# Kernel optimization log

Hardware: AMD Instinct MI355X
Metric: run time of the kernel (lower is better)

## Reference

```python
import jax, jax.numpy as jnp
import numpy as np

B, S, D_IN, D_OUT, N_EXPERTS = 8, 4096, 512, 512, 8


def setup_inputs() -> dict:
    key = jax.random.key(0)
    k1, k2, k3, k4 = jax.random.split(key, 4)
    x = jax.random.normal(k1, (B, S, D_IN), dtype=jnp.float32)
    partitions = jax.random.randint(k2, (B, S), 0, N_EXPERTS, dtype=jnp.int32)
    # per-branch nn.Linear weights: [n, out_features, in_features], kaiming-ish scale
    W = jax.random.normal(k3, (N_EXPERTS, D_OUT, D_IN), dtype=jnp.float32) * 0.03
    b = jax.random.normal(k4, (N_EXPERTS, D_OUT), dtype=jnp.float32) * 0.01
    return {"x": x, "partitions": partitions, "W": W, "b": b}


def reference(x, partitions, W, b):
    # Hard token partition -> per-branch linear -> scatter combine.
    # Equivalent math to dynamic_partition + branch Linear + dynamic_stitch:
    # out[t] = x[t] @ W[p[t]].T + b[p[t]]
    in_shape = x.shape
    xf = x.reshape(-1, in_shape[-1])          # [T, d_in]
    p = partitions.reshape(-1)                # [T]
    # Compute all-expert outputs, then select per-token expert (vectorized
    # replacement for the variable-size per-partition GEMM loop).
    y = jnp.einsum('td,eod->teo', xf, W) + b[None, :, :]   # [T, n, d_out]
    out = jnp.take_along_axis(y, p[:, None, None], axis=1)[:, 0, :]  # [T, d_out]
    return out.reshape(in_shape[:-1] + (W.shape[1],))
```

## Files before the change

kernel.cpp:

```cpp
#include <hip/hip_runtime.h>
#include <hip/hip_bf16.h>

#define N_EXPERTS 8
#define T_TOKENS 32768
#define D 512
#define TILE 128
#define BK 64
#define MAX_MTILES 264
#define SORT_CAP (MAX_MTILES * TILE)
#define NT (D / TILE)
#define GRID_WG (NT * MAX_MTILES)

typedef __bf16 bf16x8 __attribute__((ext_vector_type(8)));
typedef float  f32x4  __attribute__((ext_vector_type(4)));
typedef unsigned short u16x8 __attribute__((ext_vector_type(8)));

__device__ __forceinline__ unsigned short f2bf(float f) {
    unsigned int u = __float_as_uint(f);
    u += 0x7FFFu + ((u >> 16) & 1u);
    return (unsigned short)(u >> 16);
}

__device__ __forceinline__ u16x8 ldcvt8(const float* p) {
    float4 a = *(const float4*)p;
    float4 b = *(const float4*)(p + 4);
    u16x8 o;
    o[0] = f2bf(a.x); o[1] = f2bf(a.y); o[2] = f2bf(a.z); o[3] = f2bf(a.w);
    o[4] = f2bf(b.x); o[5] = f2bf(b.y); o[6] = f2bf(b.z); o[7] = f2bf(b.w);
    return o;
}

__device__ __forceinline__ void gl2lds16(const void* g, void* l) {
    __builtin_amdgcn_global_load_lds(
        (const __attribute__((address_space(1))) void*)g,
        (__attribute__((address_space(3))) void*)l, 16, 0, 0);
}

__global__ void hist_kernel(const int* __restrict__ p, int* __restrict__ counts) {
    __shared__ int h[N_EXPERTS];
    int tid = threadIdx.x;
    if (tid < N_EXPERTS) h[tid] = 0;
    __syncthreads();
    for (int t = blockIdx.x * blockDim.x + tid; t < T_TOKENS; t += gridDim.x * blockDim.x)
        atomicAdd(&h[p[t]], 1);
    __syncthreads();
    if (tid < N_EXPERTS) atomicAdd(&counts[tid], h[tid]);
}

__global__ void scatter_kernel(const int* __restrict__ p, const int* __restrict__ counts,
                               int* __restrict__ fill, int* __restrict__ sorted) {
    __shared__ int lcount[N_EXPERTS];
    __shared__ int lbase[N_EXPERTS];
    __shared__ int sps[N_EXPERTS];
    int tid = threadIdx.x;
    if (tid < N_EXPERTS) lcount[tid] = 0;
    __syncthreads();
    int t = blockIdx.x * blockDim.x + tid;
    int e = 0, lrank = 0;
    if (t < T_TOKENS) {
        e = p[t];
        lrank = atomicAdd(&lcount[e], 1);
    }
    __syncthreads();
    if (tid < N_EXPERTS)
        lbase[tid] = (lcount[tid] > 0) ? atomicAdd(&fill[tid], lcount[tid]) : 0;
    if (tid == 0) {
        int acc = 0;
#pragma unroll
        for (int i = 0; i < N_EXPERTS; i++) {
            sps[i] = acc;
            acc += (counts[i] + TILE - 1) & ~(TILE - 1);
        }
    }
    __syncthreads();
    if (t < T_TOKENS)
        sorted[sps[e] + lbase[e] + lrank] = t;
}

__global__ __launch_bounds__(256) void convert_w(
        const float* __restrict__ W, unsigned short* __restrict__ Wb) {
    size_t i = (size_t)(blockIdx.x * 256 + threadIdx.x) * 8;
    *(u16x8*)&Wb[i] = ldcvt8(W + i);
}

__global__ __launch_bounds__(256, 4) void moe_gemm_fused(
        const float* __restrict__ x, const unsigned short* __restrict__ Wb,
        const float* __restrict__ bias, const int* __restrict__ counts,
        const int* __restrict__ sorted, float* __restrict__ out) {
    __shared__ int s_idx[TILE];
    __shared__ unsigned short sA[TILE * BK];
    __shared__ unsigned short sB[TILE * BK];

    int lid = blockIdx.x;
    int v = (lid & 7) * (GRID_WG / 8) + (lid >> 3);
    int bm = v >> 2, bn = v & 3;
    int row0 = bm * TILE;

    int acc_off = 0, e = 0, found = 0;
#pragma unroll
    for (int i = 0; i < N_EXPERTS; i++) {
        int c = (counts[i] + TILE - 1) & ~(TILE - 1);
        if (!found && row0 < acc_off + c) { e = i; found = 1; }
        acc_off += c;
    }
    if (row0 >= acc_off) return;

    int tid = threadIdx.x;
    if (tid < TILE) s_idx[tid] = sorted[row0 + tid];
    __syncthreads();

    int wave = tid >> 6, lane = tid & 63;
    int wm = (wave >> 1) * 64, wn = (wave & 1) * 64;
    int lrow = lane & 15, lq = lane >> 4;
    int srow = lane >> 3, scol = lane & 7, swz = scol ^ srow;

    const float* aptr[4];
#pragma unroll
    for (int t = 0; t < 4; t++) {
        int tok = s_idx[wave * 32 + t * 8 + srow];
        aptr[t] = x + (size_t)(tok < 0 ? 0 : tok) * D + swz * 8;
    }
    const unsigned short* gB = Wb + (size_t)e * D * D
                             + (size_t)(bn * TILE + wave * 32 + srow) * D + swz * 8;
    unsigned short* lB = sB + (wave * 32) * BK;

    u16x8 pa[4];
#pragma unroll
    for (int t = 0; t < 4; t++) pa[t] = ldcvt8(aptr[t]);

    f32x4 acc[4][4];
#pragma unroll
    for (int i = 0; i < 4; i++)
#pragma unroll
        for (int j = 0; j < 4; j++)
            acc[i][j] = (f32x4){0.f, 0.f, 0.f, 0.f};

    for (int kk = 0; kk < D; kk += BK) {
        __syncthreads();
#pragma unroll
        for (int t = 0; t < 4; t++) {
            int r = wave * 32 + t * 8 + srow;
            *(u16x8*)&sA[r * BK + scol * 8] = pa[t];
        }
#pragma unroll
        for (int t = 0; t < 4; t++)
            gl2lds16(gB + (size_t)(t * 8) * D + kk, lB + t * 8 * BK);
        if (kk + BK < D) {
#pragma unroll
            for (int t = 0; t < 4; t++) pa[t] = ldcvt8(aptr[t] + kk + BK);
        }
        __syncthreads();
#pragma unroll
        for (int ks = 0; ks < 2; ks++) {
            bf16x8 af[4], bfr[4];
#pragma unroll
            for (int i = 0; i < 4; i++) {
                int row = wm + 16 * i + lrow;
                int cb = (ks * 4 + lq) ^ (lrow & 7);
                af[i] = *(const bf16x8*)&sA[row * BK + cb * 8];
            }
#pragma unroll
            for (int j = 0; j < 4; j++) {
                int row = wn + 16 * j + lrow;
                int cb = (ks * 4 + lq) ^ (lrow & 7);
                bfr[j] = *(const bf16x8*)&sB[row * BK + cb * 8];
            }
#pragma unroll
            for (int i = 0; i < 4; i++)
#pragma unroll
                for (int j = 0; j < 4; j++)
                    acc[i][j] = __builtin_amdgcn_mfma_f32_16x16x32_bf16(
                        af[i], bfr[j], acc[i][j], 0, 0, 0);
        }
    }

#pragma unroll
    for (int j = 0; j < 4; j++) {
        int ng = bn * TILE + wn + 16 * j + lrow;
        float bv = bias[e * D + ng];
#pragma unroll
        for (int i = 0; i < 4; i++) {
#pragma unroll
            for (int r = 0; r < 4; r++) {
                int mrow = wm + 16 * i + lq * 4 + r;
                int tok = s_idx[mrow];
                if (tok >= 0)
                    out[(size_t)tok * D + ng] = acc[i][j][r] + bv;
            }
        }
    }
}

__global__ __launch_bounds__(256) void moe_gemm_f32(
        const float* __restrict__ x, const float* __restrict__ W,
        const float* __restrict__ bias, const int* __restrict__ counts,
        const int* __restrict__ sorted, float* __restrict__ out) {
    __shared__ int s_idx[TILE];
    __shared__ unsigned short sA[TILE][BK + 8];
    __shared__ unsigned short sB[TILE][BK + 8];

    int bm = blockIdx.x, bn = blockIdx.y;
    int row0 = bm * TILE;
    int acc_off = 0, e = 0, found = 0;
#pragma unroll
    for (int i = 0; i < N_EXPERTS; i++) {
        int c = (counts[i] + TILE - 1) & ~(TILE - 1);
        if (!found && row0 < acc_off + c) { e = i; found = 1; }
        acc_off += c;
    }
    if (row0 >= acc_off) return;

    int tid = threadIdx.x;
    if (tid < TILE) s_idx[tid] = sorted[row0 + tid];
    __syncthreads();

    const float* Wb = W + (size_t)e * D * D + (size_t)(bn * TILE) * D;

    f32x4 acc[4][4];
#pragma unroll
    for (int i = 0; i < 4; i++)
#pragma unroll
        for (int j = 0; j < 4; j++)
            acc[i][j] = (f32x4){0.f, 0.f, 0.f, 0.f};

    int wave = tid >> 6, lane = tid & 63;
    int wm = (wave >> 1) * 64, wn = (wave & 1) * 64;
    int lrow = lane & 15, lq = lane >> 4;

    for (int kk = 0; kk < D; kk += BK) {
#pragma unroll
        for (int i = 0; i < 8; i++) {
            int flat = tid + i * 256;
            int r = flat >> 4, c = (flat & 15) << 2;
            int tok = s_idx[r];
            float4 v = make_float4(0.f, 0.f, 0.f, 0.f);
            if (tok >= 0) v = *(const float4*)(x + (size_t)tok * D + kk + c);
            ushort4 w4;
            w4.x = f2bf(v.x); w4.y = f2bf(v.y); w4.z = f2bf(v.z); w4.w = f2bf(v.w);
            *(ushort4*)&sA[r][c] = w4;
        }
#pragma unroll
        for (int i = 0; i < 8; i++) {
            int flat = tid + i * 256;
            int r = flat >> 4, c = (flat & 15) << 2;
            float4 v = *(const float4*)(Wb + (size_t)r * D + kk + c);
            ushort4 w4;
            w4.x = f2bf(v.x); w4.y = f2bf(v.y); w4.z = f2bf(v.z); w4.w = f2bf(v.w);
            *(ushort4*)&sB[r][c] = w4;
        }
        __syncthreads();
#pragma unroll
        for (int ks = 0; ks < 2; ks++) {
            bf16x8 af[4], bfr[4];
#pragma unroll
            for (int i = 0; i < 4; i++)
                af[i] = *(const bf16x8*)&sA[wm + 16 * i + lrow][ks * 32 + lq * 8];
#pragma unroll
            for (int j = 0; j < 4; j++)
                bfr[j] = *(const bf16x8*)&sB[wn + 16 * j + lrow][ks * 32 + lq * 8];
#pragma unroll
            for (int i = 0; i < 4; i++)
#pragma unroll
                for (int j = 0; j < 4; j++)
                    acc[i][j] = __builtin_amdgcn_mfma_f32_16x16x32_bf16(
                        af[i], bfr[j], acc[i][j], 0, 0, 0);
        }
        __syncthreads();
    }

#pragma unroll
    for (int j = 0; j < 4; j++) {
        int ng = bn * TILE + wn + 16 * j + lrow;
        float bv = bias[e * D + ng];
#pragma unroll
        for (int i = 0; i < 4; i++) {
#pragma unroll
            for (int r = 0; r < 4; r++) {
                int mrow = wm + 16 * i + lq * 4 + r;
                int tok = s_idx[mrow];
                if (tok >= 0)
                    out[(size_t)tok * D + ng] = acc[i][j][r] + bv;
            }
        }
    }
}

extern "C" void kernel_launch(void* const* d_in, const int* in_sizes, int n_in,
                              void* d_out, int out_size, void* d_ws, size_t ws_size,
                              hipStream_t stream) {
    const float* x    = (const float*)d_in[0];
    const int*   part = (const int*)d_in[1];
    const float* W    = (const float*)d_in[2];
    const float* b    = (const float*)d_in[3];
    float* out = (float*)d_out;

    const size_t wb_elems = (size_t)N_EXPERTS * D * D;
    const size_t fast_bytes = wb_elems * 2 + SORT_CAP * 4 + 16 * 4;

    if (ws_size >= fast_bytes) {
        unsigned short* Wb = (unsigned short*)d_ws;
        int* sorted = (int*)(Wb + wb_elems);
        int* counts = sorted + SORT_CAP;
        int* fill   = counts + N_EXPERTS;

        hipMemsetAsync(sorted, 0xFF, SORT_CAP * sizeof(int), stream);
        hipMemsetAsync(counts, 0, 2 * N_EXPERTS * sizeof(int), stream);

        hist_kernel<<<64, 256, 0, stream>>>(part, counts);
        scatter_kernel<<<(T_TOKENS + 255) / 256, 256, 0, stream>>>(part, counts, fill, sorted);
        convert_w<<<(int)(wb_elems / 8 / 256), 256, 0, stream>>>(W, Wb);
        moe_gemm_fused<<<GRID_WG, 256, 0, stream>>>(x, Wb, b, counts, sorted, out);
    } else {
        int* sorted = (int*)d_ws;
        int* counts = sorted + SORT_CAP;
        int* fill   = counts + N_EXPERTS;

        hipMemsetAsync(sorted, 0xFF, SORT_CAP * sizeof(int), stream);
        hipMemsetAsync(counts, 0, 2 * N_EXPERTS * sizeof(int), stream);

        hist_kernel<<<64, 256, 0, stream>>>(part, counts);
        scatter_kernel<<<(T_TOKENS + 255) / 256, 256, 0, stream>>>(part, counts, fill, sorted);

        dim3 grid(MAX_MTILES, D / TILE);
        moe_gemm_f32<<<grid, 256, 0, stream>>>(x, W, b, counts, sorted, out);
    }
}
```

Measured before the change: 188.1 us.

## Fuse routing prep into one kernel and double-buffer weight tiles in GEMM

Replaces the separate histogram, scatter and weight-conversion kernels, plus the large sorted-index memset, with a single prep kernel. Each expert now gets a fixed T_TOKENS-sized slot range with an atomic fill counter, so the histogram pass and prefix sum are no longer needed. The GEMM now indexes blocks by expert and local tile, double-buffers the B tile in LDS, and prefetches the next A slice during compute using explicit barriers and scheduling fences. Occupancy is lowered to 3 blocks per CU, and the grid grows to 8192 blocks, most of which exit immediately; the L2-friendly block swizzle is also dropped.

```diff
diff --git a/kernel.cpp b/kernel.cpp
--- a/kernel.cpp
+++ b/kernel.cpp
@@ -6,10 +6,11 @@
 #define D 512
 #define TILE 128
 #define BK 64
-#define MAX_MTILES 264
-#define SORT_CAP (MAX_MTILES * TILE)
-#define NT (D / TILE)
-#define GRID_WG (NT * MAX_MTILES)
+#define NT 4
+#define LT_MAX 256
+#define GEMM_GRID (N_EXPERTS * LT_MAX * NT)
+#define SCATTER_BLOCKS (T_TOKENS / 256)
+#define CONVW_BLOCKS ((N_EXPERTS * D * D) / (8 * 256))
 
 typedef __bf16 bf16x8 __attribute__((ext_vector_type(8)));
 typedef float  f32x4  __attribute__((ext_vector_type(4)));
@@ -21,9 +22,7 @@
     return (unsigned short)(u >> 16);
 }
 
-__device__ __forceinline__ u16x8 ldcvt8(const float* p) {
-    float4 a = *(const float4*)p;
-    float4 b = *(const float4*)(p + 4);
+__device__ __forceinline__ u16x8 cvt8(float4 a, float4 b) {
     u16x8 o;
     o[0] = f2bf(a.x); o[1] = f2bf(a.y); o[2] = f2bf(a.z); o[3] = f2bf(a.w);
     o[4] = f2bf(b.x); o[5] = f2bf(b.y); o[6] = f2bf(b.z); o[7] = f2bf(b.w);
@@ -36,77 +35,53 @@
         (__attribute__((address_space(3))) void*)l, 16, 0, 0);
 }
 
-__global__ void hist_kernel(const int* __restrict__ p, int* __restrict__ counts) {
-    __shared__ int h[N_EXPERTS];
+__global__ __launch_bounds__(256) void prep_kernel(
+        const int* __restrict__ p, int* __restrict__ fill, int* __restrict__ sorted,
+        const float* __restrict__ W, unsigned short* __restrict__ Wb) {
+    int bid = blockIdx.x;
     int tid = threadIdx.x;
-    if (tid < N_EXPERTS) h[tid] = 0;
-    __syncthreads();
-    for (int t = blockIdx.x * blockDim.x + tid; t < T_TOKENS; t += gridDim.x * blockDim.x)
-        atomicAdd(&h[p[t]], 1);
-    __syncthreads();
-    if (tid < N_EXPERTS) atomicAdd(&counts[tid], h[tid]);
-}
-
-__global__ void scatter_kernel(const int* __restrict__ p, const int* __restrict__ counts,
-                               int* __restrict__ fill, int* __restrict__ sorted) {
-    __shared__ int lcount[N_EXPERTS];
-    __shared__ int lbase[N_EXPERTS];
-    __shared__ int sps[N_EXPERTS];
-    int tid = threadIdx.x;
-    if (tid < N_EXPERTS) lcount[tid] = 0;
-    __syncthreads();
-    int t = blockIdx.x * blockDim.x + tid;
-    int e = 0, lrank = 0;
-    if (t < T_TOKENS) {
-        e = p[t];
-        lrank = atomicAdd(&lcount[e], 1);
-    }
-    __syncthreads();
-    if (tid < N_EXPERTS)
-        lbase[tid] = (lcount[tid] > 0) ? atomicAdd(&fill[tid], lcount[tid]) : 0;
-    if (tid == 0) {
-        int acc = 0;
-#pragma unroll
-        for (int i = 0; i < N_EXPERTS; i++) {
-            sps[i] = acc;
-            acc += (counts[i] + TILE - 1) & ~(TILE - 1);
-        }
-    }
-    __syncthreads();
-    if (t < T_TOKENS)
-        sorted[sps[e] + lbase[e] + lrank] = t;
-}
-
-__global__ __launch_bounds__(256) void convert_w(
-        const float* __restrict__ W, unsigned short* __restrict__ Wb) {
-    size_t i = (size_t)(blockIdx.x * 256 + threadIdx.x) * 8;
-    *(u16x8*)&Wb[i] = ldcvt8(W + i);
-}
-
-__global__ __launch_bounds__(256, 4) void moe_gemm_fused(
+    if (bid < SCATTER_BLOCKS) {
+        __shared__ int lcount[N_EXPERTS];
+        __shared__ int lbase[N_EXPERTS];
+        if (tid < N_EXPERTS) lcount[tid] = 0;
+        __syncthreads();
+        int t = bid * 256 + tid;
+        int e = p[t];
+        int lrank = atomicAdd(&lcount[e], 1);
+        __syncthreads();
+        if (tid < N_EXPERTS)
+            lbase[tid] = (lcount[tid] > 0) ? atomicAdd(&fill[tid], lcount[tid]) : 0;
+        __syncthreads();
+        sorted[e * T_TOKENS + (lbase[e] + 1 + lrank)] = t;
+    } else {
+        size_t i = ((size_t)(bid - SCATTER_BLOCKS) * 256 + tid) * 8;
+        float4 a = *(const float4*)(W + i);
+        float4 b = *(const float4*)(W + i + 4);
+        *(u16x8*)&Wb[i] = cvt8(a, b);
+    }
+}
+
+__global__ __launch_bounds__(256, 3) void moe_gemm_fused(
         const float* __restrict__ x, const unsigned short* __restrict__ Wb,
-        const float* __restrict__ bias, const int* __restrict__ counts,
+        const float* __restrict__ bias, const int* __restrict__ fill,
         const int* __restrict__ sorted, float* __restrict__ out) {
     __shared__ int s_idx[TILE];
     __shared__ unsigned short sA[TILE * BK];
-    __shared__ unsigned short sB[TILE * BK];
-
-    int lid = blockIdx.x;
-    int v = (lid & 7) * (GRID_WG / 8) + (lid >> 3);
-    int bm = v >> 2, bn = v & 3;
-    int row0 = bm * TILE;
-
-    int acc_off = 0, e = 0, found = 0;
-#pragma unroll
-    for (int i = 0; i < N_EXPERTS; i++) {
-        int c = (counts[i] + TILE - 1) & ~(TILE - 1);
-        if (!found && row0 < acc_off + c) { e = i; found = 1; }
-        acc_off += c;
-    }
-    if (row0 >= acc_off) return;
+    __shared__ unsigned short sB[2][TILE * BK];
+
+    int bid = blockIdx.x;
+    int e = bid & 7;
+    int cnt = fill[e] + 1;
+    int j = bid >> 3;
+    int lt = j >> 2, bn = j & 3;
+    int row0 = lt * TILE;
+    if (row0 >= cnt) return;
 
     int tid = threadIdx.x;
-    if (tid < TILE) s_idx[tid] = sorted[row0 + tid];
+    if (tid < TILE) {
+        int r = row0 + tid;
+        s_idx[tid] = (r < cnt) ? sorted[e * T_TOKENS + r] : -1;
+    }
     __syncthreads();
 
     int wave = tid >> 6, lane = tid & 63;
@@ -122,34 +97,54 @@
     }
     const unsigned short* gB = Wb + (size_t)e * D * D
                              + (size_t)(bn * TILE + wave * 32 + srow) * D + swz * 8;
-    unsigned short* lB = sB + (wave * 32) * BK;
-
-    u16x8 pa[4];
-#pragma unroll
-    for (int t = 0; t < 4; t++) pa[t] = ldcvt8(aptr[t]);
+
+#pragma unroll
+    for (int t = 0; t < 4; t++)
+        gl2lds16(gB + (size_t)(t * 8) * D, &sB[0][(wave * 32 + t * 8) * BK]);
+    __builtin_amdgcn_sched_barrier(0);
+    float4 pa[8];
+#pragma unroll
+    for (int t = 0; t < 4; t++) {
+        pa[2 * t]     = *(const float4*)(aptr[t]);
+        pa[2 * t + 1] = *(const float4*)(aptr[t] + 4);
+    }
 
     f32x4 acc[4][4];
 #pragma unroll
     for (int i = 0; i < 4; i++)
 #pragma unroll
-        for (int j = 0; j < 4; j++)
-            acc[i][j] = (f32x4){0.f, 0.f, 0.f, 0.f};
-
-    for (int kk = 0; kk < D; kk += BK) {
-        __syncthreads();
+        for (int j2 = 0; j2 < 4; j2++)
+            acc[i][j2] = (f32x4){0.f, 0.f, 0.f, 0.f};
+
+#pragma unroll
+    for (int step = 0; step < 8; step++) {
+        const int kk = step * BK;
+        asm volatile("s_waitcnt lgkmcnt(0)" ::: "memory");
+        __builtin_amdgcn_s_barrier();
+        __builtin_amdgcn_sched_barrier(0);
 #pragma unroll
         for (int t = 0; t < 4; t++) {
-            int r = wave * 32 + t * 8 + srow;
-            *(u16x8*)&sA[r * BK + scol * 8] = pa[t];
-        }
-#pragma unroll
-        for (int t = 0; t < 4; t++)
-            gl2lds16(gB + (size_t)(t * 8) * D + kk, lB + t * 8 * BK);
-        if (kk + BK < D) {
-#pragma unroll
-            for (int t = 0; t < 4; t++) pa[t] = ldcvt8(aptr[t] + kk + BK);
-        }
-        __syncthreads();
+            u16x8 av = cvt8(pa[2 * t], pa[2 * t + 1]);
+            *(u16x8*)&sA[(wave * 32 + t * 8 + srow) * BK + scol * 8] = av;
+        }
+        __builtin_amdgcn_sched_barrier(0);
+        if (step < 7) {
+#pragma unroll
+            for (int t = 0; t < 4; t++)
+                gl2lds16(gB + (size_t)(t * 8) * D + kk + BK,
+                         &sB[(step + 1) & 1][(wave * 32 + t * 8) * BK]);
+            __builtin_amdgcn_sched_barrier(0);
+#pragma unroll
+            for (int t = 0; t < 4; t++) {
+                pa[2 * t]     = *(const float4*)(aptr[t] + kk + BK);
+                pa[2 * t + 1] = *(const float4*)(aptr[t] + kk + BK + 4);
+            }
+            __builtin_amdgcn_sched_barrier(0);
+        }
+        asm volatile("s_waitcnt lgkmcnt(0)" ::: "memory");
+        __builtin_amdgcn_s_barrier();
+        __builtin_amdgcn_sched_barrier(0);
+        const unsigned short* sBc = sB[step & 1];
 #pragma unroll
         for (int ks = 0; ks < 2; ks++) {
             bf16x8 af[4], bfr[4];
@@ -160,23 +155,23 @@
                 af[i] = *(const bf16x8*)&sA[row * BK + cb * 8];
             }
 #pragma unroll
-            for (int j = 0; j < 4; j++) {
-                int row = wn + 16 * j + lrow;
+            for (int j2 = 0; j2 < 4; j2++) {
+                int row = wn + 16 * j2 + lrow;
                 int cb = (ks * 4 + lq) ^ (lrow & 7);
-                bfr[j] = *(const bf16x8*)&sB[row * BK + cb * 8];
+                bfr[j2] = *(const bf16x8*)&sBc[row * BK + cb * 8];
             }
 #pragma unroll
             for (int i = 0; i < 4; i++)
 #pragma unroll
-                for (int j = 0; j < 4; j++)
-                    acc[i][j] = __builtin_amdgcn_mfma_f32_16x16x32_bf16(
-                        af[i], bfr[j], acc[i][j], 0, 0, 0);
-        }
-    }
-
-#pragma unroll
-    for (int j = 0; j < 4; j++) {
-        int ng = bn * TILE + wn + 16 * j + lrow;
+                for (int j2 = 0; j2 < 4; j2++)
+                    acc[i][j2] = __builtin_amdgcn_mfma_f32_16x16x32_bf16(
+                        af[i], bfr[j2], acc[i][j2], 0, 0, 0);
+        }
+    }
+
+#pragma unroll
+    for (int j2 = 0; j2 < 4; j2++) {
+        int ng = bn * TILE + wn + 16 * j2 + lrow;
         float bv = bias[e * D + ng];
 #pragma unroll
         for (int i = 0; i < 4; i++) {
@@ -185,7 +180,7 @@
                 int mrow = wm + 16 * i + lq * 4 + r;
                 int tok = s_idx[mrow];
                 if (tok >= 0)
-                    out[(size_t)tok * D + ng] = acc[i][j][r] + bv;
+                    out[(size_t)tok * D + ng] = acc[i][j2][r] + bv;
             }
         }
     }
@@ -193,25 +188,25 @@
 
 __global__ __launch_bounds__(256) void moe_gemm_f32(
         const float* __restrict__ x, const float* __restrict__ W,
-        const float* __restrict__ bias, const int* __restrict__ counts,
+        const float* __restrict__ bias, const int* __restrict__ fill,
         const int* __restrict__ sorted, float* __restrict__ out) {
     __shared__ int s_idx[TILE];
     __shared__ unsigned short sA[TILE][BK + 8];
     __shared__ unsigned short sB[TILE][BK + 8];
 
-    int bm = blockIdx.x, bn = blockIdx.y;
-    int row0 = bm * TILE;
-    int acc_off = 0, e = 0, found = 0;
-#pragma unroll
-    for (int i = 0; i < N_EXPERTS; i++) {
-        int c = (counts[i] + TILE - 1) & ~(TILE - 1);
-        if (!found && row0 < acc_off + c) { e = i; found = 1; }
-        acc_off += c;
-    }
-    if (row0 >= acc_off) return;
+    int bid = blockIdx.x;
+    int e = bid & 7;
+    int cnt = fill[e] + 1;
+    int j = bid >> 3;
+    int lt = j >> 2, bn = j & 3;
+    int row0 = lt * TILE;
+    if (row0 >= cnt) return;
 
     int tid = threadIdx.x;
-    if (tid < TILE) s_idx[tid] = sorted[row0 + tid];
+    if (tid < TILE) {
+        int r = row0 + tid;
+        s_idx[tid] = (r < cnt) ? sorted[e * T_TOKENS + r] : -1;
+    }
     __syncthreads();
 
     const float* Wb = W + (size_t)e * D * D + (size_t)(bn * TILE) * D;
@@ -220,8 +215,8 @@
 #pragma unroll
     for (int i = 0; i < 4; i++)
 #pragma unroll
-        for (int j = 0; j < 4; j++)
-            acc[i][j] = (f32x4){0.f, 0.f, 0.f, 0.f};
+        for (int j2 = 0; j2 < 4; j2++)
+            acc[i][j2] = (f32x4){0.f, 0.f, 0.f, 0.f};
 
     int wave = tid >> 6, lane = tid & 63;
     int wm = (wave >> 1) * 64, wn = (wave & 1) * 64;
@@ -256,21 +251,21 @@
             for (int i = 0; i < 4; i++)
                 af[i] = *(const bf16x8*)&sA[wm + 16 * i + lrow][ks * 32 + lq * 8];
 #pragma unroll
-            for (int j = 0; j < 4; j++)
-                bfr[j] = *(const bf16x8*)&sB[wn + 16 * j + lrow][ks * 32 + lq * 8];
+            for (int j2 = 0; j2 < 4; j2++)
+                bfr[j2] = *(const bf16x8*)&sB[wn + 16 * j2 + lrow][ks * 32 + lq * 8];
 #pragma unroll
             for (int i = 0; i < 4; i++)
 #pragma unroll
-                for (int j = 0; j < 4; j++)
-                    acc[i][j] = __builtin_amdgcn_mfma_f32_16x16x32_bf16(
-                        af[i], bfr[j], acc[i][j], 0, 0, 0);
-        }
-        __syncthreads();
-    }
-
-#pragma unroll
-    for (int j = 0; j < 4; j++) {
-        int ng = bn * TILE + wn + 16 * j + lrow;
+                for (int j2 = 0; j2 < 4; j2++)
+                    acc[i][j2] = __builtin_amdgcn_mfma_f32_16x16x32_bf16(
+                        af[i], bfr[j2], acc[i][j2], 0, 0, 0);
+        }
+        __syncthreads();
+    }
+
+#pragma unroll
+    for (int j2 = 0; j2 < 4; j2++) {
+        int ng = bn * TILE + wn + 16 * j2 + lrow;
         float bv = bias[e * D + ng];
 #pragma unroll
         for (int i = 0; i < 4; i++) {
@@ -279,7 +274,7 @@
                 int mrow = wm + 16 * i + lq * 4 + r;
                 int tok = s_idx[mrow];
                 if (tok >= 0)
-                    out[(size_t)tok * D + ng] = acc[i][j][r] + bv;
+                    out[(size_t)tok * D + ng] = acc[i][j2][r] + bv;
             }
         }
     }
@@ -294,34 +289,27 @@
     const float* b    = (const float*)d_in[3];
     float* out = (float*)d_out;
 
-    const size_t wb_elems = (size_t)N_EXPERTS * D * D;
-    const size_t fast_bytes = wb_elems * 2 + SORT_CAP * 4 + 16 * 4;
+    const size_t wb_elems     = (size_t)N_EXPERTS * D * D;
+    const size_t sorted_elems = (size_t)N_EXPERTS * T_TOKENS;
+    const size_t fast_bytes   = wb_elems * 2 + (sorted_elems + 8) * 4;
+    const size_t slow_bytes   = (sorted_elems + 8) * 4;
 
     if (ws_size >= fast_bytes) {
         unsigned short* Wb = (unsigned short*)d_ws;
         int* sorted = (int*)(Wb + wb_elems);
-        int* counts = sorted + SORT_CAP;
-        int* fill   = counts + N_EXPERTS;
-
-        hipMemsetAsync(sorted, 0xFF, SORT_CAP * sizeof(int), stream);
-        hipMemsetAsync(counts, 0, 2 * N_EXPERTS * sizeof(int), stream);
-
-        hist_kernel<<<64, 256, 0, stream>>>(part, counts);
-        scatter_kernel<<<(T_TOKENS + 255) / 256, 256, 0, stream>>>(part, counts, fill, sorted);
-        convert_w<<<(int)(wb_elems / 8 / 256), 256, 0, stream>>>(W, Wb);
-        moe_gemm_fused<<<GRID_WG, 256, 0, stream>>>(x, Wb, b, counts, sorted, out);
-    } else {
+        int* fill   = sorted + sorted_elems;
+
+        hipMemsetAsync(fill, 0xFF, N_EXPERTS * sizeof(int), stream);
+        prep_kernel<<<SCATTER_BLOCKS + CONVW_BLOCKS, 256, 0, stream>>>(
+            part, fill, sorted, W, Wb);
+        moe_gemm_fused<<<GEMM_GRID, 256, 0, stream>>>(x, Wb, b, fill, sorted, out);
+    } else if (ws_size >= slow_bytes) {
         int* sorted = (int*)d_ws;
-        int* counts = sorted + SORT_CAP;
-        int* fill   = counts + N_EXPERTS;
-
-        hipMemsetAsync(sorted, 0xFF, SORT_CAP * sizeof(int), stream);
-        hipMemsetAsync(counts, 0, 2 * N_EXPERTS * sizeof(int), stream);
-
-        hist_kernel<<<64, 256, 0, stream>>>(part, counts);
-        scatter_kernel<<<(T_TOKENS + 255) / 256, 256, 0, stream>>>(part, counts, fill, sorted);
-
-        dim3 grid(MAX_MTILES, D / TILE);
-        moe_gemm_f32<<<grid, 256, 0, stream>>>(x, W, b, counts, sorted, out);
-    }
-}
+        int* fill   = sorted + sorted_elems;
+
+        hipMemsetAsync(fill, 0xFF, N_EXPERTS * sizeof(int), stream);
+        prep_kernel<<<SCATTER_BLOCKS, 256, 0, stream>>>(
+            part, fill, sorted, W, (unsigned short*)nullptr);
+        moe_gemm_f32<<<GEMM_GRID, 256, 0, stream>>>(x, W, b, fill, sorted, out);
+    }
+}
```

After: 167.9 us. 10.7% less time.
